# Performance work log

Hardware: AMD Instinct MI355X
Metric: run time of the kernel (lower is better)

The kernel has to match this reference:

```python
import jax, jax.numpy as jnp
import numpy as np

SCALE = 0.08838834764831845  # 1/sqrt(output_dim=128)


def setup_inputs() -> dict:
    key = jax.random.key(0)
    ks = jax.random.split(key, 7)
    N, D, H, E = 4096, 1024, 8, 128
    s = 0.02
    return {
        "X": jax.random.normal(ks[0], (N, D), jnp.float32),
        "Wq": jax.random.normal(ks[1], (H, D, E), jnp.float32) * s,
        "bq": jax.random.normal(ks[2], (H, E), jnp.float32) * s,
        "Wk": jax.random.normal(ks[3], (H, D, E), jnp.float32) * s,
        "bk": jax.random.normal(ks[4], (H, E), jnp.float32) * s,
        "Wv": jax.random.normal(ks[5], (H, D, E), jnp.float32) * s,
        "bv": jax.random.normal(ks[6], (H, E), jnp.float32) * s,
    }


def reference(X, Wq, bq, Wk, bk, Wv, bv):
    # per-head projections, batched over heads: [H, N, E]
    q = jnp.einsum("nd,hde->hne", X, Wq) + bq[:, None, :]
    k = jnp.einsum("nd,hde->hne", X, Wk) + bk[:, None, :]
    v = jnp.einsum("nd,hde->hne", X, Wv) + bv[:, None, :]
    # score[h, n, m] = scale * q[h,n,:] . k[h,m,:]  ([H, N, N])
    score = SCALE * jnp.einsum("hne,hme->hnm", q, k)
    # NOTE: original uses nn.Softmax(dim=0) on the [N, N] per-head matrix,
    # i.e. normalization over the QUERY (row) axis -> axis=1 here.
    attn = jax.nn.softmax(score, axis=1)
    # z[h, n, e] = sum_m attn[h,n,m] * v[h,m,e]
    z = jnp.einsum("hnm,hme->hne", attn, v)
    # concat heads along feature dim: [N, H*E]
    H, N, E = z.shape
    Z = jnp.transpose(z, (1, 0, 2)).reshape(N, H * E)
    return jax.nn.sigmoid(Z)
```

## Files before the change

### kernel.cpp

```cpp
#include <hip/hip_runtime.h>
#include <hip/hip_bf16.h>
#include <stdint.h>

typedef __bf16 bf16_t;
typedef __bf16 bf16x4 __attribute__((ext_vector_type(4)));
typedef __bf16 bf16x8 __attribute__((ext_vector_type(8)));
typedef float f32x4 __attribute__((ext_vector_type(4)));

#define MFMA_16x16x32(A, B, C) __builtin_amdgcn_mfma_f32_16x16x32_bf16(A, B, C, 0, 0, 0)
#define EXP2(x) __builtin_amdgcn_exp2f(x)

static constexpr float kScale = 0.08838834764831845f;
static constexpr float kLog2e = 1.4426950408889634f;
static constexpr float kC1 = kScale * kLog2e;

__device__ __forceinline__ void lds_cp16(void* lds, const void* g) {
  __builtin_amdgcn_global_load_lds(
      (__attribute__((address_space(1))) void*)(uintptr_t)g,
      (__attribute__((address_space(3))) void*)(uintptr_t)lds, 16, 0, 0);
}

template <int R, int K>
__device__ __forceinline__ void stage_tile(bf16_t* lds, const bf16_t* g, int ldg, int tid) {
  constexpr int TOT = R * K;
  constexpr int CH = R * 32;
  constexpr int ITERS = TOT / 2048;
  const int wave = tid >> 6;
#pragma unroll
  for (int i = 0; i < ITERS; ++i) {
    int linear = i * 2048 + tid * 8;
    int chunk = linear / CH;
    int rem = linear % CH;
    int r = rem >> 5;
    int c = rem & 31;
    lds_cp16(lds + i * 2048 + wave * 512, g + r * ldg + chunk * 32 + c);
  }
}

__device__ __forceinline__ bf16x8 frag_ld(const bf16_t* lds_chunk, int row, int lane) {
  return *(const bf16x8*)(lds_chunk + row * 32 + ((lane >> 4) << 3));
}

__global__ void cvt_kernel(const float* __restrict__ src, bf16_t* __restrict__ dst) {
  const int i = (blockIdx.x * 256 + threadIdx.x) * 4;
  float4 v = *(const float4*)&src[i];
  bf16x4 o;
  o[0] = (bf16_t)v.x;
  o[1] = (bf16_t)v.y;
  o[2] = (bf16_t)v.z;
  o[3] = (bf16_t)v.w;
  *(bf16x4*)&dst[i] = o;
}

__global__ void transpose_f32_k(const float* __restrict__ src, bf16_t* __restrict__ dst, int R,
                                int C) {
  __shared__ alignas(16) bf16_t tile[64][72];
  const int t = threadIdx.x;
  const int mat = blockIdx.z;
  const int r0 = blockIdx.x * 64, c0 = blockIdx.y * 64;
  const float* s = src + (size_t)mat * R * C;
  bf16_t* d = dst + (size_t)mat * R * C;
  const int rl = t >> 3, cl = (t & 7) * 8;
#pragma unroll
  for (int half = 0; half < 2; ++half) {
    const int r = r0 + rl + half * 32;
    float4 a = *(const float4*)&s[(size_t)r * C + c0 + cl];
    float4 b = *(const float4*)&s[(size_t)r * C + c0 + cl + 4];
    tile[cl + 0][rl + half * 32] = (bf16_t)a.x;
    tile[cl + 1][rl + half * 32] = (bf16_t)a.y;
    tile[cl + 2][rl + half * 32] = (bf16_t)a.z;
    tile[cl + 3][rl + half * 32] = (bf16_t)a.w;
    tile[cl + 4][rl + half * 32] = (bf16_t)b.x;
    tile[cl + 5][rl + half * 32] = (bf16_t)b.y;
    tile[cl + 6][rl + half * 32] = (bf16_t)b.z;
    tile[cl + 7][rl + half * 32] = (bf16_t)b.w;
  }
  __syncthreads();
  const int cl2 = t >> 3, rl2 = (t & 7) * 8;
  *(bf16x8*)&d[(size_t)(c0 + cl2) * R + r0 + rl2] = *(const bf16x8*)&tile[cl2][rl2];
  *(bf16x8*)&d[(size_t)(c0 + cl2 + 32) * R + r0 + rl2] = *(const bf16x8*)&tile[cl2 + 32][rl2];
}

__global__ __launch_bounds__(256, 2) void proj_kernel(const bf16_t* __restrict__ X,
                                                      const bf16_t* __restrict__ Wt,
                                                      const float* __restrict__ bq,
                                                      const float* __restrict__ bk,
                                                      const float* __restrict__ bv,
                                                      bf16_t* __restrict__ qkv) {
  __shared__ alignas(16) bf16_t As[128 * 32];
  __shared__ alignas(16) bf16_t Bs[128 * 32];
  const int t = threadIdx.x, lane = t & 63, w = t >> 6;
  const int l15 = lane & 15, quad = lane >> 4;
  const int ntile = blockIdx.x, mat = blockIdx.y;
  const bf16_t* a0 = X + (size_t)ntile * 128 * 1024;
  const bf16_t* b0 = Wt + (size_t)mat * 131072;
  f32x4 acc[4][4] = {};
  const int rb = (w >> 1) * 64, cb = (w & 1) * 64;
  for (int k0 = 0; k0 < 1024; k0 += 32) {
    stage_tile<128, 32>(As, a0 + k0, 1024, t);
    stage_tile<128, 32>(Bs, b0 + k0, 1024, t);
    __syncthreads();
    bf16x8 af[4], bfr[4];
#pragma unroll
    for (int i = 0; i < 4; ++i) af[i] = frag_ld(As, rb + i * 16 + l15, lane);
#pragma unroll
    for (int j = 0; j < 4; ++j) bfr[j] = frag_ld(Bs, cb + j * 16 + l15, lane);
#pragma unroll
    for (int i = 0; i < 4; ++i)
#pragma unroll
      for (int j = 0; j < 4; ++j) acc[i][j] = MFMA_16x16x32(af[i], bfr[j], acc[i][j]);
    __syncthreads();
  }
  const int proj = mat >> 3, h = mat & 7;
  const float* bias = (proj == 0 ? bq : proj == 1 ? bk : bv) + h * 128;
  const size_t moff = (size_t)mat * 524288 + (mat >= 16 ? 4194304 : 0);
  bf16_t* outp = qkv + moff;
#pragma unroll
  for (int i = 0; i < 4; ++i) {
#pragma unroll
    for (int j = 0; j < 4; ++j) {
      const int e = cb + j * 16 + l15;
      const float bval = bias[e];
#pragma unroll
      for (int r = 0; r < 4; ++r) {
        const int n = ntile * 128 + rb + i * 16 + quad * 4 + r;
        outp[(size_t)n * 128 + e] = (bf16_t)(acc[i][j][r] + bval);
      }
    }
  }
}

__global__ void repack_qk(const bf16_t* __restrict__ src, bf16_t* __restrict__ dst) {
  __shared__ alignas(16) bf16_t S[64 * 128];
  const int t = threadIdx.x, lane = t & 63, w = t >> 6, l15 = lane & 15;
  const int h = blockIdx.x, ng = blockIdx.y;
  const bf16_t* s = src + ((size_t)h * 4096 + ng * 64) * 128;
  stage_tile<64, 128>(S, s, 128, t);
  __syncthreads();
  const int nt = ng * 4 + w;
#pragma unroll
  for (int ks = 0; ks < 4; ++ks) {
    bf16x8 f = frag_ld(S + ks * 2048, w * 16 + l15, lane);
    *(bf16x8*)&dst[(((size_t)h * 256 + nt) * 4 + ks) * 512 + lane * 8] = f;
  }
}

__global__ void repack_v(const bf16_t* __restrict__ v, bf16_t* __restrict__ Vf) {
  __shared__ alignas(16) bf16_t tile[64][72];
  const int t = threadIdx.x;
  const int h = blockIdx.z;
  const int r0 = blockIdx.x * 64, c0 = blockIdx.y * 64;
  const bf16_t* s = v + (size_t)h * 4096 * 128;
  const int rl = t >> 3, cl = (t & 7) * 8;
  bf16x8 v0 = *(const bf16x8*)&s[(size_t)(r0 + rl) * 128 + c0 + cl];
  bf16x8 v1 = *(const bf16x8*)&s[(size_t)(r0 + rl + 32) * 128 + c0 + cl];
#pragma unroll
  for (int j = 0; j < 8; ++j) {
    tile[cl + j][rl] = v0[j];
    tile[cl + j][rl + 32] = v1[j];
  }
  __syncthreads();
  const int lane = t & 63, w = t >> 6, quad = lane >> 4, l15 = lane & 15;
  const int es = (c0 >> 4) + w;
#pragma unroll
  for (int mi = 0; mi < 2; ++mi) {
    bf16x8 f = *(const bf16x8*)&tile[w * 16 + l15][mi * 32 + quad * 8];
    const int mb = (r0 >> 5) + mi;
    *(bf16x8*)&Vf[(((size_t)h * 128 + mb) * 8 + es) * 512 + lane * 8] = f;
  }
}

__global__ __launch_bounds__(256, 3) void pass_a_kernel(const bf16_t* __restrict__ Qf,
                                                        const bf16_t* __restrict__ Kf,
                                                        float* __restrict__ l2c) {
  __shared__ alignas(16) float csred[4][64];
  const int t = threadIdx.x, lane = t & 63, w = t >> 6;
  const int h = blockIdx.x, mtile = blockIdx.y;
  const bf16_t* Qh = Qf + (size_t)h * 524288;
  const bf16_t* Kh = Kf + (size_t)h * 524288;
  bf16x8 kf[4][4];
#pragma unroll
  for (int mg = 0; mg < 4; ++mg)
#pragma unroll
    for (int ks = 0; ks < 4; ++ks)
      kf[mg][ks] = *(const bf16x8*)&Kh[((size_t)(mtile * 4 + mg) * 4 + ks) * 512 + lane * 8];
  float cs[4] = {0.f, 0.f, 0.f, 0.f};
  bf16x8 af[4];
#pragma unroll
  for (int ks = 0; ks < 4; ++ks)
    af[ks] = *(const bf16x8*)&Qh[(size_t)(w * 4 + ks) * 512 + lane * 8];
  for (int it = 0; it < 64; ++it) {
    const int ntn = ((it + 1) * 4 + w) & 255;
    bf16x8 afn[4];
#pragma unroll
    for (int ks = 0; ks < 4; ++ks)
      afn[ks] = *(const bf16x8*)&Qh[((size_t)ntn * 4 + ks) * 512 + lane * 8];
#pragma unroll
    for (int mg = 0; mg < 4; ++mg) {
      f32x4 c = {0.f, 0.f, 0.f, 0.f};
#pragma unroll
      for (int ks = 0; ks < 4; ++ks) c = MFMA_16x16x32(af[ks], kf[mg][ks], c);
#pragma unroll
      for (int r = 0; r < 4; ++r) cs[mg] += EXP2(c[r] * kC1);
    }
#pragma unroll
    for (int ks = 0; ks < 4; ++ks) af[ks] = afn[ks];
  }
#pragma unroll
  for (int mg = 0; mg < 4; ++mg) {
    cs[mg] += __shfl_xor(cs[mg], 16, 64);
    cs[mg] += __shfl_xor(cs[mg], 32, 64);
  }
  if (lane < 16) {
#pragma unroll
    for (int mg = 0; mg < 4; ++mg) csred[w][mg * 16 + lane] = cs[mg];
  }
  __syncthreads();
  if (t < 64)
    l2c[(size_t)h * 4096 + mtile * 64 + t] =
        __builtin_log2f(csred[0][t] + csred[1][t] + csred[2][t] + csred[3][t]);
}

__global__ __launch_bounds__(256, 2) void pass_b_kernel(const bf16_t* __restrict__ Qf,
                                                        const bf16_t* __restrict__ Kf,
                                                        const bf16_t* __restrict__ Vf,
                                                        const float* __restrict__ l2c,
                                                        float* __restrict__ out) {
  __shared__ alignas(16) bf16_t sW_all[4][32][40];
  __shared__ alignas(16) float zred[2][4096];
  const int t = threadIdx.x, lane = t & 63, w = t >> 6;
  const int quad = lane >> 4, l15 = lane & 15;
  const int npar = w & 1, mpar = w >> 1;
  const int h = blockIdx.x, ntile = blockIdx.y;
  const bf16_t* Qh = Qf + (size_t)h * 524288;
  const bf16_t* Kh = Kf + (size_t)h * 524288;
  const bf16_t* Vh = Vf + (size_t)h * 524288;
  const float* lb = l2c + (size_t)h * 4096;
  bf16x8 qf[2][4];
#pragma unroll
  for (int nsub = 0; nsub < 2; ++nsub)
#pragma unroll
    for (int ks = 0; ks < 4; ++ks)
      qf[nsub][ks] = *(const bf16x8*)&Qh[((size_t)(ntile * 4 + npar * 2 + nsub) * 4 + ks) * 512 +
                                         lane * 8];
  bf16_t* sW = &sW_all[w][0][0];
  f32x4 zacc[2][8] = {};
  bf16x8 kf[2][4];
#pragma unroll
  for (int ms = 0; ms < 2; ++ms)
#pragma unroll
    for (int ks = 0; ks < 4; ++ks)
      kf[ms][ks] = *(const bf16x8*)&Kh[((size_t)(mpar * 2 + ms) * 4 + ks) * 512 + lane * 8];
  for (int it = 0; it < 64; ++it) {
    const int st = it * 2 + mpar;
    const int stn = (st + 2) & 127;
    bf16x8 vf[8];
#pragma unroll
    for (int es = 0; es < 8; ++es)
      vf[es] = *(const bf16x8*)&Vh[((size_t)st * 8 + es) * 512 + lane * 8];
    f32x4 g0 = *(const f32x4*)&lb[st * 32 + quad * 4];
    f32x4 g1 = *(const f32x4*)&lb[st * 32 + 16 + quad * 4];
    f32x4 cc[2][2] = {};
#pragma unroll
    for (int ks = 0; ks < 4; ++ks)
#pragma unroll
      for (int ms = 0; ms < 2; ++ms)
#pragma unroll
        for (int nsub = 0; nsub < 2; ++nsub)
          cc[ms][nsub] = MFMA_16x16x32(kf[ms][ks], qf[nsub][ks], cc[ms][nsub]);
    bf16x8 kfn[2][4];
#pragma unroll
    for (int ms = 0; ms < 2; ++ms)
#pragma unroll
      for (int ks = 0; ks < 4; ++ks)
        kfn[ms][ks] = *(const bf16x8*)&Kh[((size_t)(stn * 2 + ms) * 4 + ks) * 512 + lane * 8];
#pragma unroll
    for (int ms = 0; ms < 2; ++ms) {
      const f32x4 g = ms ? g1 : g0;
#pragma unroll
      for (int nsub = 0; nsub < 2; ++nsub) {
        bf16x4 pv;
#pragma unroll
        for (int r = 0; r < 4; ++r) pv[r] = (bf16_t)EXP2(cc[ms][nsub][r] * kC1 - g[r]);
        *(bf16x4*)&sW[(nsub * 16 + l15) * 40 + ms * 16 + quad * 4] = pv;
      }
    }
    bf16x8 pf[2];
#pragma unroll
    for (int nsub = 0; nsub < 2; ++nsub)
      pf[nsub] = *(const bf16x8*)&sW[(nsub * 16 + l15) * 40 + quad * 8];
#pragma unroll
    for (int es = 0; es < 8; ++es)
#pragma unroll
      for (int nsub = 0; nsub < 2; ++nsub)
        zacc[nsub][es] = MFMA_16x16x32(pf[nsub], vf[es], zacc[nsub][es]);
#pragma unroll
    for (int ms = 0; ms < 2; ++ms)
#pragma unroll
      for (int ks = 0; ks < 4; ++ks) kf[ms][ks] = kfn[ms][ks];
  }
  __syncthreads();
  if (mpar == 1) {
    float* dst = &zred[npar][0];
#pragma unroll
    for (int i = 0; i < 16; ++i) *(f32x4*)&dst[i * 256 + lane * 4] = zacc[i >> 3][i & 7];
  }
  __syncthreads();
  if (mpar == 0) {
    const float* src = &zred[npar][0];
#pragma unroll
    for (int nsub = 0; nsub < 2; ++nsub) {
#pragma unroll
      for (int es = 0; es < 8; ++es) {
        f32x4 o = *(const f32x4*)&src[(nsub * 8 + es) * 256 + lane * 4];
        const int e = es * 16 + l15;
#pragma unroll
        for (int r = 0; r < 4; ++r) {
          const int n = ntile * 64 + npar * 32 + nsub * 16 + quad * 4 + r;
          const float z = zacc[nsub][es][r] + o[r];
          out[(size_t)n * 1024 + h * 128 + e] = 1.f / (1.f + EXP2(-z * kLog2e));
        }
      }
    }
  }
}

extern "C" void kernel_launch(void* const* d_in, const int* in_sizes, int n_in, void* d_out,
                              int out_size, void* d_ws, size_t ws_size, hipStream_t stream) {
  (void)in_sizes;
  (void)n_in;
  (void)out_size;
  (void)ws_size;
  const float* X = (const float*)d_in[0];
  const float* Wq = (const float*)d_in[1];
  const float* bq = (const float*)d_in[2];
  const float* Wk = (const float*)d_in[3];
  const float* bk = (const float*)d_in[4];
  const float* Wv = (const float*)d_in[5];
  const float* bv = (const float*)d_in[6];
  float* out = (float*)d_out;
  char* ws = (char*)d_ws;
  bf16_t* q_rm = (bf16_t*)(ws);
  bf16_t* Kf = (bf16_t*)(ws);
  bf16_t* k_rm = (bf16_t*)(ws + 8388608);
  float* l2c = (float*)(ws + 8388608);
  bf16_t* Xb = (bf16_t*)(ws + 16777216);
  bf16_t* Vf = (bf16_t*)(ws + 16777216);
  bf16_t* v_rm = (bf16_t*)(ws + 25165824);
  bf16_t* Qf = (bf16_t*)(ws + 25165824);
  bf16_t* Wt = (bf16_t*)(ws + 33554432);

  cvt_kernel<<<4096, 256, 0, stream>>>(X, Xb);
  transpose_f32_k<<<dim3(16, 2, 8), 256, 0, stream>>>(Wq, Wt + (size_t)0 * 8 * 131072, 1024, 128);
  transpose_f32_k<<<dim3(16, 2, 8), 256, 0, stream>>>(Wk, Wt + (size_t)1 * 8 * 131072, 1024, 128);
  transpose_f32_k<<<dim3(16, 2, 8), 256, 0, stream>>>(Wv, Wt + (size_t)2 * 8 * 131072, 1024, 128);
  proj_kernel<<<dim3(32, 24), 256, 0, stream>>>(Xb, Wt, bq, bk, bv, q_rm);
  repack_v<<<dim3(64, 2, 8), 256, 0, stream>>>(v_rm, Vf);
  repack_qk<<<dim3(8, 64), 256, 0, stream>>>(q_rm, Qf);
  repack_qk<<<dim3(8, 64), 256, 0, stream>>>(k_rm, Kf);
  pass_a_kernel<<<dim3(8, 64), 256, 0, stream>>>(Qf, Kf, l2c);
  pass_b_kernel<<<dim3(8, 64), 256, 0, stream>>>(Qf, Kf, Vf, l2c, out);
}
```

Baseline: 280.4 us.

## Fuse QKV repack into projection epilogue and halve attention tiles for more blocks

```diff
diff --git a/kernel.cpp b/kernel.cpp
--- a/kernel.cpp
+++ b/kernel.cpp
@@ -87,8 +87,9 @@
                                                       const float* __restrict__ bk,
                                                       const float* __restrict__ bv,
                                                       bf16_t* __restrict__ qkv) {
-  __shared__ alignas(16) bf16_t As[128 * 32];
-  __shared__ alignas(16) bf16_t Bs[128 * 32];
+  __shared__ alignas(16) char smem[34816];
+  bf16_t* As = (bf16_t*)smem;
+  bf16_t* Bs = (bf16_t*)(smem + 8192);
   const int t = threadIdx.x, lane = t & 63, w = t >> 6;
   const int l15 = lane & 15, quad = lane >> 4;
   const int ntile = blockIdx.x, mat = blockIdx.y;
@@ -113,121 +114,107 @@
   }
   const int proj = mat >> 3, h = mat & 7;
   const float* bias = (proj == 0 ? bq : proj == 1 ? bk : bv) + h * 128;
-  const size_t moff = (size_t)mat * 524288 + (mat >= 16 ? 4194304 : 0);
-  bf16_t* outp = qkv + moff;
-#pragma unroll
-  for (int i = 0; i < 4; ++i) {
-#pragma unroll
-    for (int j = 0; j < 4; ++j) {
-      const int e = cb + j * 16 + l15;
-      const float bval = bias[e];
-#pragma unroll
-      for (int r = 0; r < 4; ++r) {
-        const int n = ntile * 128 + rb + i * 16 + quad * 4 + r;
-        outp[(size_t)n * 128 + e] = (bf16_t)(acc[i][j][r] + bval);
+  bf16_t* Ct = (bf16_t*)smem;
+  bf16_t* dst = qkv + (size_t)proj * 4194304 + (size_t)h * 524288;
+  if (proj < 2) {
+#pragma unroll
+    for (int i = 0; i < 4; ++i)
+#pragma unroll
+      for (int j = 0; j < 4; ++j) {
+        const int e = cb + j * 16 + l15;
+        const float bval = bias[e];
+#pragma unroll
+        for (int r = 0; r < 4; ++r)
+          Ct[(rb + i * 16 + quad * 4 + r) * 136 + e] = (bf16_t)(acc[i][j][r] + bval);
       }
-    }
-  }
-}
-
-__global__ void repack_qk(const bf16_t* __restrict__ src, bf16_t* __restrict__ dst) {
-  __shared__ alignas(16) bf16_t S[64 * 128];
-  const int t = threadIdx.x, lane = t & 63, w = t >> 6, l15 = lane & 15;
-  const int h = blockIdx.x, ng = blockIdx.y;
-  const bf16_t* s = src + ((size_t)h * 4096 + ng * 64) * 128;
-  stage_tile<64, 128>(S, s, 128, t);
-  __syncthreads();
-  const int nt = ng * 4 + w;
-#pragma unroll
-  for (int ks = 0; ks < 4; ++ks) {
-    bf16x8 f = frag_ld(S + ks * 2048, w * 16 + l15, lane);
-    *(bf16x8*)&dst[(((size_t)h * 256 + nt) * 4 + ks) * 512 + lane * 8] = f;
-  }
-}
-
-__global__ void repack_v(const bf16_t* __restrict__ v, bf16_t* __restrict__ Vf) {
-  __shared__ alignas(16) bf16_t tile[64][72];
-  const int t = threadIdx.x;
-  const int h = blockIdx.z;
-  const int r0 = blockIdx.x * 64, c0 = blockIdx.y * 64;
-  const bf16_t* s = v + (size_t)h * 4096 * 128;
-  const int rl = t >> 3, cl = (t & 7) * 8;
-  bf16x8 v0 = *(const bf16x8*)&s[(size_t)(r0 + rl) * 128 + c0 + cl];
-  bf16x8 v1 = *(const bf16x8*)&s[(size_t)(r0 + rl + 32) * 128 + c0 + cl];
-#pragma unroll
-  for (int j = 0; j < 8; ++j) {
-    tile[cl + j][rl] = v0[j];
-    tile[cl + j][rl + 32] = v1[j];
-  }
-  __syncthreads();
-  const int lane = t & 63, w = t >> 6, quad = lane >> 4, l15 = lane & 15;
-  const int es = (c0 >> 4) + w;
-#pragma unroll
-  for (int mi = 0; mi < 2; ++mi) {
-    bf16x8 f = *(const bf16x8*)&tile[w * 16 + l15][mi * 32 + quad * 8];
-    const int mb = (r0 >> 5) + mi;
-    *(bf16x8*)&Vf[(((size_t)h * 128 + mb) * 8 + es) * 512 + lane * 8] = f;
-  }
-}
-
-__global__ __launch_bounds__(256, 3) void pass_a_kernel(const bf16_t* __restrict__ Qf,
+    __syncthreads();
+#pragma unroll
+    for (int u = 0; u < 2; ++u) {
+      const int nt = w * 2 + u;
+#pragma unroll
+      for (int ks = 0; ks < 4; ++ks) {
+        bf16x8 f = *(const bf16x8*)&Ct[(nt * 16 + l15) * 136 + ks * 32 + quad * 8];
+        *(bf16x8*)&dst[(((size_t)(ntile * 8 + nt)) * 4 + ks) * 512 + lane * 8] = f;
+      }
+    }
+  } else {
+#pragma unroll
+    for (int i = 0; i < 4; ++i)
+#pragma unroll
+      for (int j = 0; j < 4; ++j) {
+        const int e = cb + j * 16 + l15;
+        const float bval = bias[e];
+        bf16x4 pv;
+#pragma unroll
+        for (int r = 0; r < 4; ++r) pv[r] = (bf16_t)(acc[i][j][r] + bval);
+        *(bf16x4*)&Ct[e * 136 + rb + i * 16 + quad * 4] = pv;
+      }
+    __syncthreads();
+#pragma unroll
+    for (int es = 0; es < 8; ++es) {
+      bf16x8 f = *(const bf16x8*)&Ct[(es * 16 + l15) * 136 + w * 32 + quad * 8];
+      *(bf16x8*)&dst[(((size_t)(ntile * 4 + w)) * 8 + es) * 512 + lane * 8] = f;
+    }
+  }
+}
+
+__global__ __launch_bounds__(256, 4) void pass_a_kernel(const bf16_t* __restrict__ Qf,
                                                         const bf16_t* __restrict__ Kf,
                                                         float* __restrict__ l2c) {
-  __shared__ alignas(16) float csred[4][64];
+  __shared__ alignas(16) float csred[4][32];
   const int t = threadIdx.x, lane = t & 63, w = t >> 6;
+  const int quad = lane >> 4, l15 = lane & 15;
   const int h = blockIdx.x, mtile = blockIdx.y;
   const bf16_t* Qh = Qf + (size_t)h * 524288;
   const bf16_t* Kh = Kf + (size_t)h * 524288;
-  bf16x8 kf[4][4];
-#pragma unroll
-  for (int mg = 0; mg < 4; ++mg)
+  bf16x8 kf[8];
+#pragma unroll
+  for (int mg = 0; mg < 2; ++mg)
 #pragma unroll
     for (int ks = 0; ks < 4; ++ks)
-      kf[mg][ks] = *(const bf16x8*)&Kh[((size_t)(mtile * 4 + mg) * 4 + ks) * 512 + lane * 8];
-  float cs[4] = {0.f, 0.f, 0.f, 0.f};
+      kf[mg * 4 + ks] = *(const bf16x8*)&Kh[((mtile * 2 + mg) * 4 + ks) * 512 + lane * 8];
+  float cs0 = 0.f, cs1 = 0.f;
+  uint32_t qo = w * 2048 + lane * 8;
   bf16x8 af[4];
 #pragma unroll
-  for (int ks = 0; ks < 4; ++ks)
-    af[ks] = *(const bf16x8*)&Qh[(size_t)(w * 4 + ks) * 512 + lane * 8];
+  for (int ks = 0; ks < 4; ++ks) af[ks] = *(const bf16x8*)&Qh[qo + ks * 512];
   for (int it = 0; it < 64; ++it) {
-    const int ntn = ((it + 1) * 4 + w) & 255;
-    bf16x8 afn[4];
-#pragma unroll
-    for (int ks = 0; ks < 4; ++ks)
-      afn[ks] = *(const bf16x8*)&Qh[((size_t)ntn * 4 + ks) * 512 + lane * 8];
-#pragma unroll
-    for (int mg = 0; mg < 4; ++mg) {
-      f32x4 c = {0.f, 0.f, 0.f, 0.f};
-#pragma unroll
-      for (int ks = 0; ks < 4; ++ks) c = MFMA_16x16x32(af[ks], kf[mg][ks], c);
-#pragma unroll
-      for (int r = 0; r < 4; ++r) cs[mg] += EXP2(c[r] * kC1);
-    }
-#pragma unroll
-    for (int ks = 0; ks < 4; ++ks) af[ks] = afn[ks];
-  }
-#pragma unroll
-  for (int mg = 0; mg < 4; ++mg) {
-    cs[mg] += __shfl_xor(cs[mg], 16, 64);
-    cs[mg] += __shfl_xor(cs[mg], 32, 64);
-  }
+    f32x4 c0 = {0.f, 0.f, 0.f, 0.f}, c1 = {0.f, 0.f, 0.f, 0.f};
+#pragma unroll
+    for (int ks = 0; ks < 4; ++ks) {
+      c0 = MFMA_16x16x32(af[ks], kf[ks], c0);
+      c1 = MFMA_16x16x32(af[ks], kf[4 + ks], c1);
+    }
+    qo += 8192;
+#pragma unroll
+    for (int ks = 0; ks < 4; ++ks) af[ks] = *(const bf16x8*)&Qh[qo + ks * 512];
+#pragma unroll
+    for (int r = 0; r < 4; ++r) {
+      cs0 += EXP2(c0[r] * kC1);
+      cs1 += EXP2(c1[r] * kC1);
+    }
+  }
+  cs0 += __shfl_xor(cs0, 16, 64);
+  cs0 += __shfl_xor(cs0, 32, 64);
+  cs1 += __shfl_xor(cs1, 16, 64);
+  cs1 += __shfl_xor(cs1, 32, 64);
   if (lane < 16) {
-#pragma unroll
-    for (int mg = 0; mg < 4; ++mg) csred[w][mg * 16 + lane] = cs[mg];
+    csred[w][lane] = cs0;
+    csred[w][16 + lane] = cs1;
   }
   __syncthreads();
-  if (t < 64)
-    l2c[(size_t)h * 4096 + mtile * 64 + t] =
+  if (t < 32)
+    l2c[(size_t)h * 4096 + mtile * 32 + t] =
         __builtin_log2f(csred[0][t] + csred[1][t] + csred[2][t] + csred[3][t]);
 }
 
-__global__ __launch_bounds__(256, 2) void pass_b_kernel(const bf16_t* __restrict__ Qf,
+__global__ __launch_bounds__(256, 4) void pass_b_kernel(const bf16_t* __restrict__ Qf,
                                                         const bf16_t* __restrict__ Kf,
                                                         const bf16_t* __restrict__ Vf,
                                                         const float* __restrict__ l2c,
                                                         float* __restrict__ out) {
-  __shared__ alignas(16) bf16_t sW_all[4][32][40];
-  __shared__ alignas(16) float zred[2][4096];
+  __shared__ alignas(16) bf16_t sW_all[4][16][40];
+  __shared__ alignas(16) float zred[2][2048];
   const int t = threadIdx.x, lane = t & 63, w = t >> 6;
   const int quad = lane >> 4, l15 = lane & 15;
   const int npar = w & 1, mpar = w >> 1;
@@ -236,90 +223,64 @@
   const bf16_t* Kh = Kf + (size_t)h * 524288;
   const bf16_t* Vh = Vf + (size_t)h * 524288;
   const float* lb = l2c + (size_t)h * 4096;
-  bf16x8 qf[2][4];
-#pragma unroll
-  for (int nsub = 0; nsub < 2; ++nsub)
-#pragma unroll
-    for (int ks = 0; ks < 4; ++ks)
-      qf[nsub][ks] = *(const bf16x8*)&Qh[((size_t)(ntile * 4 + npar * 2 + nsub) * 4 + ks) * 512 +
-                                         lane * 8];
+  bf16x8 qf[4];
+#pragma unroll
+  for (int ks = 0; ks < 4; ++ks)
+    qf[ks] = *(const bf16x8*)&Qh[((ntile * 2 + npar) * 4 + ks) * 512 + lane * 8];
+  uint32_t ko = mpar * 4096 + lane * 8;
+  uint32_t vo = mpar * 4096 + lane * 8;
+  bf16x8 kf[8];
+#pragma unroll
+  for (int u = 0; u < 8; ++u) kf[u] = *(const bf16x8*)&Kh[ko + u * 512];
+  bf16x8 vf[8];
+#pragma unroll
+  for (int es = 0; es < 8; ++es) vf[es] = *(const bf16x8*)&Vh[vo + es * 512];
   bf16_t* sW = &sW_all[w][0][0];
-  f32x4 zacc[2][8] = {};
-  bf16x8 kf[2][4];
-#pragma unroll
-  for (int ms = 0; ms < 2; ++ms)
-#pragma unroll
-    for (int ks = 0; ks < 4; ++ks)
-      kf[ms][ks] = *(const bf16x8*)&Kh[((size_t)(mpar * 2 + ms) * 4 + ks) * 512 + lane * 8];
+  f32x4 zacc[8] = {};
   for (int it = 0; it < 64; ++it) {
     const int st = it * 2 + mpar;
-    const int stn = (st + 2) & 127;
-    bf16x8 vf[8];
-#pragma unroll
-    for (int es = 0; es < 8; ++es)
-      vf[es] = *(const bf16x8*)&Vh[((size_t)st * 8 + es) * 512 + lane * 8];
     f32x4 g0 = *(const f32x4*)&lb[st * 32 + quad * 4];
     f32x4 g1 = *(const f32x4*)&lb[st * 32 + 16 + quad * 4];
-    f32x4 cc[2][2] = {};
-#pragma unroll
-    for (int ks = 0; ks < 4; ++ks)
-#pragma unroll
-      for (int ms = 0; ms < 2; ++ms)
-#pragma unroll
-        for (int nsub = 0; nsub < 2; ++nsub)
-          cc[ms][nsub] = MFMA_16x16x32(kf[ms][ks], qf[nsub][ks], cc[ms][nsub]);
-    bf16x8 kfn[2][4];
-#pragma unroll
-    for (int ms = 0; ms < 2; ++ms)
-#pragma unroll
-      for (int ks = 0; ks < 4; ++ks)
-        kfn[ms][ks] = *(const bf16x8*)&Kh[((size_t)(stn * 2 + ms) * 4 + ks) * 512 + lane * 8];
-#pragma unroll
-    for (int ms = 0; ms < 2; ++ms) {
-      const f32x4 g = ms ? g1 : g0;
-#pragma unroll
-      for (int nsub = 0; nsub < 2; ++nsub) {
-        bf16x4 pv;
-#pragma unroll
-        for (int r = 0; r < 4; ++r) pv[r] = (bf16_t)EXP2(cc[ms][nsub][r] * kC1 - g[r]);
-        *(bf16x4*)&sW[(nsub * 16 + l15) * 40 + ms * 16 + quad * 4] = pv;
-      }
-    }
-    bf16x8 pf[2];
-#pragma unroll
-    for (int nsub = 0; nsub < 2; ++nsub)
-      pf[nsub] = *(const bf16x8*)&sW[(nsub * 16 + l15) * 40 + quad * 8];
-#pragma unroll
-    for (int es = 0; es < 8; ++es)
-#pragma unroll
-      for (int nsub = 0; nsub < 2; ++nsub)
-        zacc[nsub][es] = MFMA_16x16x32(pf[nsub], vf[es], zacc[nsub][es]);
-#pragma unroll
-    for (int ms = 0; ms < 2; ++ms)
-#pragma unroll
-      for (int ks = 0; ks < 4; ++ks) kf[ms][ks] = kfn[ms][ks];
+    f32x4 cc0 = {0.f, 0.f, 0.f, 0.f}, cc1 = {0.f, 0.f, 0.f, 0.f};
+#pragma unroll
+    for (int ks = 0; ks < 4; ++ks) {
+      cc0 = MFMA_16x16x32(kf[ks], qf[ks], cc0);
+      cc1 = MFMA_16x16x32(kf[4 + ks], qf[ks], cc1);
+    }
+    ko += 8192;
+#pragma unroll
+    for (int u = 0; u < 8; ++u) kf[u] = *(const bf16x8*)&Kh[ko + u * 512];
+    bf16x4 p0, p1;
+#pragma unroll
+    for (int r = 0; r < 4; ++r) {
+      p0[r] = (bf16_t)EXP2(cc0[r] * kC1 - g0[r]);
+      p1[r] = (bf16_t)EXP2(cc1[r] * kC1 - g1[r]);
+    }
+    *(bf16x4*)&sW[l15 * 40 + quad * 4] = p0;
+    *(bf16x4*)&sW[l15 * 40 + 16 + quad * 4] = p1;
+    bf16x8 pf = *(const bf16x8*)&sW[l15 * 40 + quad * 8];
+#pragma unroll
+    for (int es = 0; es < 8; ++es) zacc[es] = MFMA_16x16x32(pf, vf[es], zacc[es]);
+    vo += 8192;
+#pragma unroll
+    for (int es = 0; es < 8; ++es) vf[es] = *(const bf16x8*)&Vh[vo + es * 512];
   }
   __syncthreads();
   if (mpar == 1) {
-    float* dst = &zred[npar][0];
-#pragma unroll
-    for (int i = 0; i < 16; ++i) *(f32x4*)&dst[i * 256 + lane * 4] = zacc[i >> 3][i & 7];
+#pragma unroll
+    for (int es = 0; es < 8; ++es) *(f32x4*)&zred[npar][es * 256 + lane * 4] = zacc[es];
   }
   __syncthreads();
   if (mpar == 0) {
-    const float* src = &zred[npar][0];
-#pragma unroll
-    for (int nsub = 0; nsub < 2; ++nsub) {
-#pragma unroll
-      for (int es = 0; es < 8; ++es) {
-        f32x4 o = *(const f32x4*)&src[(nsub * 8 + es) * 256 + lane * 4];
-        const int e = es * 16 + l15;
-#pragma unroll
-        for (int r = 0; r < 4; ++r) {
-          const int n = ntile * 64 + npar * 32 + nsub * 16 + quad * 4 + r;
-          const float z = zacc[nsub][es][r] + o[r];
-          out[(size_t)n * 1024 + h * 128 + e] = 1.f / (1.f + EXP2(-z * kLog2e));
-        }
+#pragma unroll
+    for (int es = 0; es < 8; ++es) {
+      f32x4 o = *(const f32x4*)&zred[npar][es * 256 + lane * 4];
+      const int e = es * 16 + l15;
+#pragma unroll
+      for (int r = 0; r < 4; ++r) {
+        const int n = ntile * 32 + npar * 16 + quad * 4 + r;
+        const float z = zacc[es][r] + o[r];
+        out[(size_t)n * 1024 + h * 128 + e] = 1.f / (1.f + EXP2(-z * kLog2e));
       }
     }
   }
@@ -340,24 +301,18 @@
   const float* bv = (const float*)d_in[6];
   float* out = (float*)d_out;
   char* ws = (char*)d_ws;
-  bf16_t* q_rm = (bf16_t*)(ws);
-  bf16_t* Kf = (bf16_t*)(ws);
-  bf16_t* k_rm = (bf16_t*)(ws + 8388608);
-  float* l2c = (float*)(ws + 8388608);
-  bf16_t* Xb = (bf16_t*)(ws + 16777216);
+  bf16_t* Qf = (bf16_t*)(ws);
+  bf16_t* Xb = (bf16_t*)(ws + 25165824);
+  bf16_t* Wt = (bf16_t*)(ws + 33554432);
+  float* l2c = (float*)(ws + 39845888);
+  bf16_t* Kf = (bf16_t*)(ws + 8388608);
   bf16_t* Vf = (bf16_t*)(ws + 16777216);
-  bf16_t* v_rm = (bf16_t*)(ws + 25165824);
-  bf16_t* Qf = (bf16_t*)(ws + 25165824);
-  bf16_t* Wt = (bf16_t*)(ws + 33554432);
 
   cvt_kernel<<<4096, 256, 0, stream>>>(X, Xb);
   transpose_f32_k<<<dim3(16, 2, 8), 256, 0, stream>>>(Wq, Wt + (size_t)0 * 8 * 131072, 1024, 128);
   transpose_f32_k<<<dim3(16, 2, 8), 256, 0, stream>>>(Wk, Wt + (size_t)1 * 8 * 131072, 1024, 128);
   transpose_f32_k<<<dim3(16, 2, 8), 256, 0, stream>>>(Wv, Wt + (size_t)2 * 8 * 131072, 1024, 128);
-  proj_kernel<<<dim3(32, 24), 256, 0, stream>>>(Xb, Wt, bq, bk, bv, q_rm);
-  repack_v<<<dim3(64, 2, 8), 256, 0, stream>>>(v_rm, Vf);
-  repack_qk<<<dim3(8, 64), 256, 0, stream>>>(q_rm, Qf);
-  repack_qk<<<dim3(8, 64), 256, 0, stream>>>(k_rm, Kf);
-  pass_a_kernel<<<dim3(8, 64), 256, 0, stream>>>(Qf, Kf, l2c);
-  pass_b_kernel<<<dim3(8, 64), 256, 0, stream>>>(Qf, Kf, Vf, l2c, out);
-}
+  proj_kernel<<<dim3(32, 24), 256, 0, stream>>>(Xb, Wt, bq, bk, bv, Qf);
+  pass_a_kernel<<<dim3(8, 128), 256, 0, stream>>>(Qf, Kf, l2c);
+  pass_b_kernel<<<dim3(8, 128), 256, 0, stream>>>(Qf, Kf, Vf, l2c, out);
+}
```

Result: slower. 344.8 us (+23.0%).
